# Kernel optimization log

Measured on AMD Instinct MI355X. Metric: run time of the kernel, lower is better.

## Reference

```python
import jax, jax.numpy as jnp
import numpy as np

N = 50000
E = 800000
F_IN = 256
F_OUT = 128
ALPHA = 0.2  # leaky relu negative slope


def setup_inputs() -> dict:
    key = jax.random.key(0)
    k1, k2, k3, k4 = jax.random.split(key, 4)
    x = jax.random.normal(k1, (N, F_IN), dtype=jnp.float32)
    edge_index = jax.random.randint(k2, (2, E), 0, N, dtype=jnp.int64 if jax.config.jax_enable_x64 else jnp.int32)
    # xavier_normal gain=1.414
    W = jax.random.normal(k3, (F_IN, F_OUT), dtype=jnp.float32) * (1.414 * np.sqrt(2.0 / (F_IN + F_OUT)))
    a = jax.random.normal(k4, (2 * F_OUT, 2 * F_OUT), dtype=jnp.float32) * (1.414 * np.sqrt(2.0 / (4 * F_OUT)))
    return {"x": x, "edge_index": edge_index, "W": W, "a": a}


def reference(x, edge_index, W, a):
    n = x.shape[0]
    src = edge_index[0]  # rows of sparse adj
    dst = edge_index[1]  # cols of sparse adj
    h = x @ W  # [N, F_out]
    hs = h[src]  # [E, F_out] gather
    hd = h[dst]  # [E, F_out] gather
    # att_type == 'mx':
    # (a @ edge_h).sum(0) == a.sum(0) @ edge_h where edge_h = cat(hs, hd).T
    asum = a.sum(0)  # [2*F_out]
    lin = hs @ asum[:F_OUT] + hd @ asum[F_OUT:]  # [E]
    conv = (hs * hd).sum(axis=1)  # [E]
    z = lin * jax.nn.sigmoid(conv)
    edge_e = jnp.exp(-jnp.where(z >= 0, z, ALPHA * z))  # exp(-leakyrelu(z))
    # sparse spmm: rowsum (a @ ones) and aggregate (a @ h); dropout p=0 (eval)
    e_rowsum = jax.ops.segment_sum(edge_e, src, num_segments=n) + 1e-8  # [N]
    h_prime = jax.ops.segment_sum(edge_e[:, None] * hd, src, num_segments=n)  # [N, F_out]
    h_prime = h_prime / e_rowsum[:, None]
    return jax.nn.elu(h_prime)  # concat=True
```

## Files before the change

kernel.cpp:

```cpp
#include <hip/hip_runtime.h>

#define NF_IN 256
#define NF 128
#define NEG_SLOPE 0.2f
#define BUCKET 64
#define CAP 12288
#define CH 4096

typedef float f32x4 __attribute__((ext_vector_type(4)));
typedef __bf16 bf16x8 __attribute__((ext_vector_type(8)));
typedef short short8 __attribute__((ext_vector_type(8)));
typedef _Float16 half8 __attribute__((ext_vector_type(8)));
typedef _Float16 half2v __attribute__((ext_vector_type(2)));
struct H2x4 { half2v h[4]; };

__device__ __forceinline__ short bf16_rtne(float f) {
    unsigned u = __float_as_uint(f);
    u += 0x7fffu + ((u >> 16) & 1u);
    return (short)(u >> 16);
}

__global__ __launch_bounds__(256) void stage_pre(const float* __restrict__ a,
                                                 const float* __restrict__ W,
                                                 const int* __restrict__ srcp,
                                                 const int* __restrict__ dstp,
                                                 float* __restrict__ av,
                                                 short* __restrict__ Wt,
                                                 unsigned* __restrict__ gcount,
                                                 unsigned* __restrict__ ebuf,
                                                 int E, int nbuck) {
    __shared__ unsigned pr_pairs[CH];
    __shared__ unsigned pr_ord[CH];
    __shared__ unsigned char pr_bkt[CH];
    __shared__ int pr_hist[128], pr_lstart[128], pr_loff[128], pr_gbase[128];

    const int tid = threadIdx.x;
    const int bid = blockIdx.x;

    if (bid < 8) {
        float s = 0.f;
        const int r0 = bid * 32;
        for (int r = 0; r < 32; ++r) s += a[(size_t)(r0 + r) * (2 * NF) + tid];
        atomicAdd(&av[tid], s);
        return;
    }
    if (bid < 136) {
        const int i = (bid - 8) * 256 + tid;
        const int k = i >> 7, c = i & 127;
        const int t = k >> 5, lg = (k >> 3) & 3, e = k & 7;
        const int q = c >> 4, col = c & 15;
        const float w = W[i];
        const unsigned b = __float_as_uint(w);
        const int base = t * 8192 + q * 512 + lg * 128 + col * 8 + e;
        Wt[base] = (short)(b >> 16);
        Wt[base + 4096] = bf16_rtne(w - __uint_as_float(b & 0xffff0000u));
        return;
    }

    const int e0 = (bid - 136) * CH;
    const int nE = min(CH, E - e0);
    if (nE <= 0) return;

    if (tid < 128) pr_hist[tid] = 0;
    __syncthreads();

    const int nE4 = nE >> 2;
    for (int i = tid; i < nE4; i += 256) {
        const int4 s4 = ((const int4*)(srcp + e0))[i];
        const int4 d4 = ((const int4*)(dstp + e0))[i];
        pr_pairs[i * 4 + 0] = (unsigned)(s4.x & 0xFFFF) | ((unsigned)(d4.x & 0xFFFF) << 16);
        pr_pairs[i * 4 + 1] = (unsigned)(s4.y & 0xFFFF) | ((unsigned)(d4.y & 0xFFFF) << 16);
        pr_pairs[i * 4 + 2] = (unsigned)(s4.z & 0xFFFF) | ((unsigned)(d4.z & 0xFFFF) << 16);
        pr_pairs[i * 4 + 3] = (unsigned)(s4.w & 0xFFFF) | ((unsigned)(d4.w & 0xFFFF) << 16);
        atomicAdd(&pr_hist[s4.x >> 9], 1);
        atomicAdd(&pr_hist[s4.y >> 9], 1);
        atomicAdd(&pr_hist[s4.z >> 9], 1);
        atomicAdd(&pr_hist[s4.w >> 9], 1);
    }
    __syncthreads();

    if (tid == 0) {
        int run = 0;
        for (int b = 0; b < nbuck; ++b) {
            pr_lstart[b] = run;
            pr_loff[b] = run;
            run += pr_hist[b];
        }
    }
    __syncthreads();

    if (tid < nbuck) {
        pr_gbase[tid] = (int)atomicAdd(&gcount[tid], (unsigned)pr_hist[tid]);
        const int st = pr_lstart[tid], cnt = pr_hist[tid];
        for (int j = 0; j < cnt; ++j) pr_bkt[st + j] = (unsigned char)tid;
    }
    __syncthreads();

    for (int i = tid; i < nE; i += 256) {
        const unsigned pv = pr_pairs[i];
        const int b = (int)(pv & 0xFFFF) >> 9;
        const int pos = atomicAdd(&pr_loff[b], 1);
        pr_ord[pos] = pv;
    }
    __syncthreads();

    for (int i = tid; i < nE; i += 256) {
        const int b = pr_bkt[i];
        const long gi = (long)pr_gbase[b] + (i - pr_lstart[b]);
        if (gi < CAP) ebuf[(size_t)b * CAP + gi] = pr_ord[i];
    }
}

__global__ __launch_bounds__(256) void stage_projfill(
        const float* __restrict__ x, const short* __restrict__ Wt,
        const float* __restrict__ av, _Float16* __restrict__ h16,
        float* __restrict__ scs, float* __restrict__ scd, int n, int nProj,
        const unsigned* __restrict__ gcount, const unsigned* __restrict__ ebuf,
        int* __restrict__ deg, unsigned short* __restrict__ nbr) {
    __shared__ short bts[2][8192];

    const int tid = threadIdx.x;

    if (blockIdx.x >= nProj) {
        const int b = blockIdx.x - nProj;
        const int nb0 = b << 9;
        const int nn = min(512, n - nb0);
        if (nn <= 0) return;
        int* deg_l = (int*)&bts[0][0];
        for (int i = tid; i < 512; i += 256) deg_l[i] = 0;

        const unsigned* reg = (const unsigned*)(nbr + ((size_t)nb0 << 6));
        unsigned acc = 0;
        const int words = nn << 5;
        for (int i = tid; i < words; i += 256) acc += reg[i];
        asm volatile("" :: "v"(acc));
        __syncthreads();

        int cnt = (int)gcount[b];
        if (cnt > CAP) cnt = CAP;
        for (int i = tid; i < cnt; i += 256) {
            const unsigned pv = ebuf[(size_t)b * CAP + i];
            const int s = (int)(pv & 0xFFFF);
            const int d = (int)(pv >> 16);
            const int k = atomicAdd(&deg_l[s - nb0], 1);
            if (k < BUCKET) nbr[((size_t)s << 6) + k] = (unsigned short)d;
        }
        __syncthreads();
        for (int i = tid; i < nn; i += 256) deg[nb0 + i] = deg_l[i];
        return;
    }

    const int lane = tid & 63;
    const int wv = tid >> 6;
    const int l15 = lane & 15;
    const int lg = lane >> 4;
    const int rbase = blockIdx.x * 64 + wv * 16;

    int arow = rbase + l15;
    if (arow >= n) arow = n - 1;
    const float* xr = x + (size_t)arow * NF_IN + lg * 8;

    short8 ah[8], al[8];
    #pragma unroll
    for (int t = 0; t < 8; ++t) {
        const float4 u0 = *(const float4*)(xr + t * 32);
        const float4 u1 = *(const float4*)(xr + t * 32 + 4);
        const float xs[8] = {u0.x, u0.y, u0.z, u0.w, u1.x, u1.y, u1.z, u1.w};
        #pragma unroll
        for (int e = 0; e < 8; ++e) {
            const unsigned b = __float_as_uint(xs[e]);
            ah[t][e] = (short)(b >> 16);
            al[t][e] = bf16_rtne(xs[e] - __uint_as_float(b & 0xffff0000u));
        }
    }

    f32x4 acc[8];
    #pragma unroll
    for (int q = 0; q < 8; ++q) acc[q] = (f32x4){0.f, 0.f, 0.f, 0.f};

    #define STAGE(t_, b_)                                                        \
        do {                                                                     \
            const short* gt_ = Wt + (size_t)(t_) * 8192;                         \
            _Pragma("unroll")                                                    \
            for (int i_ = 0; i_ < 4; ++i_) {                                     \
                const int ch_ = wv * 256 + i_ * 64;                              \
                __builtin_amdgcn_global_load_lds(                                \
                    (const __attribute__((address_space(1))) void*)              \
                        (gt_ + (size_t)(ch_ + lane) * 8),                        \
                    (__attribute__((address_space(3))) void*)&bts[b_][ch_ * 8],  \
                    16, 0, 0);                                                   \
            }                                                                    \
        } while (0)

    STAGE(0, 0);

    #pragma unroll
    for (int t = 0; t < 8; ++t) {
        __syncthreads();
        if (t < 7) STAGE(t + 1, (t + 1) & 1);
        const short* Bs = &bts[t & 1][0];
        const int boff = lg * 128 + l15 * 8;
        const bf16x8 ahv = __builtin_bit_cast(bf16x8, ah[t]);
        const bf16x8 alv = __builtin_bit_cast(bf16x8, al[t]);
        #pragma unroll
        for (int q = 0; q < 8; ++q) {
            const short8 bh = *(const short8*)(Bs + q * 512 + boff);
            const short8 bl = *(const short8*)(Bs + 4096 + q * 512 + boff);
            const bf16x8 bhv = __builtin_bit_cast(bf16x8, bh);
            const bf16x8 blv = __builtin_bit_cast(bf16x8, bl);
            acc[q] = __builtin_amdgcn_mfma_f32_16x16x32_bf16(ahv, bhv, acc[q], 0, 0, 0);
            acc[q] = __builtin_amdgcn_mfma_f32_16x16x32_bf16(alv, bhv, acc[q], 0, 0, 0);
            acc[q] = __builtin_amdgcn_mfma_f32_16x16x32_bf16(ahv, blv, acc[q], 0, 0, 0);
        }
    }
    #undef STAGE

    float avA[8], avB[8];
    #pragma unroll
    for (int q = 0; q < 8; ++q) {
        avA[q] = av[q * 16 + l15];
        avB[q] = av[NF + q * 16 + l15];
    }

    #pragma unroll
    for (int r = 0; r < 4; ++r) {
        float ps = 0.f, pd = 0.f;
        #pragma unroll
        for (int q = 0; q < 8; ++q) {
            ps += acc[q][r] * avA[q];
            pd += acc[q][r] * avB[q];
        }
        #pragma unroll
        for (int m_ = 1; m_ <= 8; m_ <<= 1) {
            ps += __shfl_xor(ps, m_, 64);
            pd += __shfl_xor(pd, m_, 64);
        }
        const int row = rbase + lg * 4 + r;
        if (row < n) {
            _Float16* hp = h16 + (size_t)row * NF;
            #pragma unroll
            for (int q = 0; q < 8; ++q) hp[q * 16 + l15] = (_Float16)acc[q][r];
            if (l15 == 0) { scs[row] = ps; scd[row] = pd; }
        }
    }
}

__global__ __launch_bounds__(256) void stage_agg(const _Float16* __restrict__ h16,
                                                 const unsigned short* __restrict__ nbr,
                                                 const int* __restrict__ deg,
                                                 const float* __restrict__ scs,
                                                 const float* __restrict__ scd,
                                                 float* __restrict__ out, int n) {
    const int node = (blockIdx.x * blockDim.x + threadIdx.x) >> 6;
    if (node >= n) return;
    const int lane = threadIdx.x & 63;
    const int qq = lane & 7;
    const int sub = lane >> 3;

    const half8* hself = (const half8*)(h16 + (size_t)node * NF + qq * 16);
    const H2x4 pa0 = __builtin_bit_cast(H2x4, hself[0]);
    const H2x4 pa1 = __builtin_bit_cast(H2x4, hself[1]);

    const float lbase = scs[node];
    const int org = node << 6;
    int dg = deg[node];
    if (dg > BUCKET) dg = BUCKET;

    float t[16];
    #pragma unroll
    for (int e = 0; e < 16; ++e) t[e] = 0.f;
    float zsum = 0.f;

    if (dg > 0) {
        float lA, lB, lC;
        half8 a0, a1, b0, b1, c0, c1;
        {
            const int iA = (int)nbr[org + ((sub < dg) ? sub : 0)];
            lA = scd[iA];
            const half8* hA = (const half8*)(h16 + (size_t)iA * NF + qq * 16);
            a0 = hA[0]; a1 = hA[1];
        }
        lB = 0.f; b0 = a0; b1 = a1;
        if (8 < dg) {
            const int jj = 8 + sub;
            const int iB = (int)nbr[org + ((jj < dg) ? jj : 0)];
            lB = scd[iB];
            const half8* hB = (const half8*)(h16 + (size_t)iB * NF + qq * 16);
            b0 = hB[0]; b1 = hB[1];
        }

        for (int j = 0; j < dg; j += 8) {
            lC = 0.f; c0 = b0; c1 = b1;
            if (j + 16 < dg) {
                const int jj = j + 16 + sub;
                const int iC = (int)nbr[org + ((jj < dg) ? jj : 0)];
                lC = scd[iC];
                const half8* hC = (const half8*)(h16 + (size_t)iC * NF + qq * 16);
                c0 = hC[0]; c1 = hC[1];
            }

            float cv = 0.f;
#if __has_builtin(__builtin_amdgcn_fdot2)
            {
                const H2x4 qa0 = __builtin_bit_cast(H2x4, a0);
                const H2x4 qa1 = __builtin_bit_cast(H2x4, a1);
                #pragma unroll
                for (int i = 0; i < 4; ++i)
                    cv = __builtin_amdgcn_fdot2(pa0.h[i], qa0.h[i], cv, false);
                #pragma unroll
                for (int i = 0; i < 4; ++i)
                    cv = __builtin_amdgcn_fdot2(pa1.h[i], qa1.h[i], cv, false);
            }
#else
            {
                const H2x4 qa0 = __builtin_bit_cast(H2x4, a0);
                const H2x4 qa1 = __builtin_bit_cast(H2x4, a1);
                #pragma unroll
                for (int i = 0; i < 4; ++i) {
                    cv += (float)pa0.h[i][0] * (float)qa0.h[i][0];
                    cv += (float)pa0.h[i][1] * (float)qa0.h[i][1];
                    cv += (float)pa1.h[i][0] * (float)qa1.h[i][0];
                    cv += (float)pa1.h[i][1] * (float)qa1.h[i][1];
                }
            }
#endif
            #pragma unroll
            for (int m = 4; m >= 1; m >>= 1) cv += __shfl_xor(cv, m, 64);

            float qv[16];
            #pragma unroll
            for (int e = 0; e < 8; ++e) { qv[e] = (float)a0[e]; qv[8 + e] = (float)a1[e]; }

            const float gate = 1.0f / (1.0f + __expf(-cv));
            const float zz = (lbase + lA) * gate;
            const float zr = (zz >= 0.f) ? zz : NEG_SLOPE * zz;
            float wt = __expf(-zr);
            if (j + sub >= dg) wt = 0.f;

            #pragma unroll
            for (int e = 0; e < 16; ++e) t[e] += wt * qv[e];
            zsum += wt;

            lA = lB; a0 = b0; a1 = b1;
            lB = lC; b0 = c0; b1 = c1;
        }
    }

    #pragma unroll
    for (int m = 8; m <= 32; m <<= 1) zsum += __shfl_xor(zsum, m, 64);

    const int b0_ = sub & 1, b1_ = (sub >> 1) & 1, b2_ = (sub >> 2) & 1;
    float u[8];
    #pragma unroll
    for (int i = 0; i < 8; ++i) {
        const int alo = ((i >> 1) << 2) | (i & 1);
        const float ka = t[alo], kb = t[alo + 2];
        const float keep = b0_ ? kb : ka;
        const float send = b0_ ? ka : kb;
        u[i] = keep + __shfl_xor(send, 8, 64);
    }
    float v[4];
    #pragma unroll
    for (int j = 0; j < 4; ++j) {
        const int alo = ((j >> 1) << 2) | (j & 1);
        const float ka = u[alo], kb = u[alo + 2];
        const float keep = b1_ ? kb : ka;
        const float send = b1_ ? ka : kb;
        v[j] = keep + __shfl_xor(send, 16, 64);
    }
    float w0, w1;
    {
        const float ka = v[0], kb = v[2];
        const float keep = b2_ ? kb : ka, send = b2_ ? ka : kb;
        w0 = keep + __shfl_xor(send, 32, 64);
    }
    {
        const float ka = v[1], kb = v[3];
        const float keep = b2_ ? kb : ka, send = b2_ ? ka : kb;
        w1 = keep + __shfl_xor(send, 32, 64);
    }

    const float norm = 1.0f / (zsum + 1e-8f);
    float y0 = w0 * norm, y1 = w1 * norm;
    y0 = (y0 > 0.f) ? y0 : (__expf(y0) - 1.f);
    y1 = (y1 > 0.f) ? y1 : (__expf(y1) - 1.f);
    *(float2*)(out + (size_t)node * NF + qq * 16 + sub * 2) = make_float2(y0, y1);
}

extern "C" void kernel_launch(void* const* d_in, const int* in_sizes, int n_in,
                              void* d_out, int out_size, void* d_ws, size_t ws_size,
                              hipStream_t stream) {
    const float* x = (const float*)d_in[0];
    const int* ei = (const int*)d_in[1];
    const float* W = (const float*)d_in[2];
    const float* a = (const float*)d_in[3];
    float* out = (float*)d_out;

    const int n = in_sizes[0] / NF_IN;
    const int E = in_sizes[1] / 2;
    const int* srcp = ei;
    const int* dstp = ei + E;

    char* w = (char*)d_ws;
    _Float16* h16 = (_Float16*)w; w += (size_t)n * NF * 2;
    float* scs = (float*)w;   w += (size_t)n * 4;
    float* scd = (float*)w;   w += (size_t)n * 4;
    float* av = (float*)w;    w += 256 * 4;
    unsigned* gcount = (unsigned*)w; w += 128 * 4;
    int* deg = (int*)w;       w += (size_t)n * 4;
    unsigned short* nbr = (unsigned short*)w; w += (size_t)n * BUCKET * 2;
    short* Wt = (short*)w;    w += (size_t)8 * 8192 * 2 * 2;
    unsigned* ebuf = (unsigned*)w;
    const int nbuck = (n + 511) >> 9;
    w += (size_t)nbuck * CAP * 4;

    const int NB1 = (E + CH - 1) / CH;
    const int nProj = (n + 63) / 64;

    hipMemsetAsync(av, 0, (256 + 128) * 4, stream);

    stage_pre<<<136 + NB1, 256, 0, stream>>>(a, W, srcp, dstp, av, Wt,
                                             gcount, ebuf, E, nbuck);
    stage_projfill<<<nProj + nbuck, 256, 0, stream>>>(
        x, Wt, av, h16, scs, scd, n, nProj, gcount, ebuf, deg, nbr);
    stage_agg<<<((size_t)n * 64 + 255) / 256, 256, 0, stream>>>(h16, nbr, deg, scs, scd,
                                                                out, n);
}
```

Before: 178.0 us.

## Process 16 neighbors per wave iteration with 4 lanes per feature row

The aggregation kernel now assigns 4 lanes per neighbor, each holding 32 fp16 features, so a wave covers 16 neighbors per iteration instead of 8. The 2-deep register prefetch becomes 1-deep, the per-edge dot-product shuffle reduction drops from 3 steps to 2, and the final transpose-reduce gains one extra shuffle level. The intent is to cut loop iterations and per-edge shuffle work for the typical degree of about 16. In exchange each lane holds 32 accumulators plus 64 fp16 inputs, which raises register pressure and can reduce occupancy.

```diff
diff --git a/kernel.cpp b/kernel.cpp
--- a/kernel.cpp
+++ b/kernel.cpp
@@ -254,49 +254,44 @@
     const int node = (blockIdx.x * blockDim.x + threadIdx.x) >> 6;
     if (node >= n) return;
     const int lane = threadIdx.x & 63;
-    const int qq = lane & 7;
-    const int sub = lane >> 3;
-
-    const half8* hself = (const half8*)(h16 + (size_t)node * NF + qq * 16);
+    const int q4 = lane & 3;
+    const int sub = lane >> 2;
+
+    const half8* hself = (const half8*)(h16 + (size_t)node * NF + q4 * 32);
     const H2x4 pa0 = __builtin_bit_cast(H2x4, hself[0]);
     const H2x4 pa1 = __builtin_bit_cast(H2x4, hself[1]);
+    const H2x4 pa2 = __builtin_bit_cast(H2x4, hself[2]);
+    const H2x4 pa3 = __builtin_bit_cast(H2x4, hself[3]);
 
     const float lbase = scs[node];
     const int org = node << 6;
     int dg = deg[node];
     if (dg > BUCKET) dg = BUCKET;
 
-    float t[16];
-    #pragma unroll
-    for (int e = 0; e < 16; ++e) t[e] = 0.f;
+    float t[32];
+    #pragma unroll
+    for (int e = 0; e < 32; ++e) t[e] = 0.f;
     float zsum = 0.f;
 
     if (dg > 0) {
-        float lA, lB, lC;
-        half8 a0, a1, b0, b1, c0, c1;
+        float lA;
+        half8 a0, a1, a2, a3;
         {
             const int iA = (int)nbr[org + ((sub < dg) ? sub : 0)];
             lA = scd[iA];
-            const half8* hA = (const half8*)(h16 + (size_t)iA * NF + qq * 16);
-            a0 = hA[0]; a1 = hA[1];
-        }
-        lB = 0.f; b0 = a0; b1 = a1;
-        if (8 < dg) {
-            const int jj = 8 + sub;
-            const int iB = (int)nbr[org + ((jj < dg) ? jj : 0)];
-            lB = scd[iB];
-            const half8* hB = (const half8*)(h16 + (size_t)iB * NF + qq * 16);
-            b0 = hB[0]; b1 = hB[1];
-        }
-
-        for (int j = 0; j < dg; j += 8) {
-            lC = 0.f; c0 = b0; c1 = b1;
+            const half8* hA = (const half8*)(h16 + (size_t)iA * NF + q4 * 32);
+            a0 = hA[0]; a1 = hA[1]; a2 = hA[2]; a3 = hA[3];
+        }
+
+        for (int j = 0; j < dg; j += 16) {
+            float lB = 0.f;
+            half8 b0 = a0, b1 = a1, b2 = a2, b3 = a3;
             if (j + 16 < dg) {
                 const int jj = j + 16 + sub;
-                const int iC = (int)nbr[org + ((jj < dg) ? jj : 0)];
-                lC = scd[iC];
-                const half8* hC = (const half8*)(h16 + (size_t)iC * NF + qq * 16);
-                c0 = hC[0]; c1 = hC[1];
+                const int iB = (int)nbr[org + ((jj < dg) ? jj : 0)];
+                lB = scd[iB];
+                const half8* hB = (const half8*)(h16 + (size_t)iB * NF + q4 * 32);
+                b0 = hB[0]; b1 = hB[1]; b2 = hB[2]; b3 = hB[3];
             }
 
             float cv = 0.f;
@@ -304,32 +299,37 @@
             {
                 const H2x4 qa0 = __builtin_bit_cast(H2x4, a0);
                 const H2x4 qa1 = __builtin_bit_cast(H2x4, a1);
+                const H2x4 qa2 = __builtin_bit_cast(H2x4, a2);
+                const H2x4 qa3 = __builtin_bit_cast(H2x4, a3);
                 #pragma unroll
-                for (int i = 0; i < 4; ++i)
+                for (int i = 0; i < 4; ++i) {
                     cv = __builtin_amdgcn_fdot2(pa0.h[i], qa0.h[i], cv, false);
-                #pragma unroll
-                for (int i = 0; i < 4; ++i)
                     cv = __builtin_amdgcn_fdot2(pa1.h[i], qa1.h[i], cv, false);
+                    cv = __builtin_amdgcn_fdot2(pa2.h[i], qa2.h[i], cv, false);
+                    cv = __builtin_amdgcn_fdot2(pa3.h[i], qa3.h[i], cv, false);
+                }
             }
 #else
             {
                 const H2x4 qa0 = __builtin_bit_cast(H2x4, a0);
                 const H2x4 qa1 = __builtin_bit_cast(H2x4, a1);
+                const H2x4 qa2 = __builtin_bit_cast(H2x4, a2);
+                const H2x4 qa3 = __builtin_bit_cast(H2x4, a3);
                 #pragma unroll
                 for (int i = 0; i < 4; ++i) {
                     cv += (float)pa0.h[i][0] * (float)qa0.h[i][0];
                     cv += (float)pa0.h[i][1] * (float)qa0.h[i][1];
                     cv += (float)pa1.h[i][0] * (float)qa1.h[i][0];
                     cv += (float)pa1.h[i][1] * (float)qa1.h[i][1];
+                    cv += (float)pa2.h[i][0] * (float)qa2.h[i][0];
+                    cv += (float)pa2.h[i][1] * (float)qa2.h[i][1];
+                    cv += (float)pa3.h[i][0] * (float)qa3.h[i][0];
+                    cv += (float)pa3.h[i][1] * (float)qa3.h[i][1];
                 }
             }
 #endif
-            #pragma unroll
-            for (int m = 4; m >= 1; m >>= 1) cv += __shfl_xor(cv, m, 64);
-
-            float qv[16];
-            #pragma unroll
-            for (int e = 0; e < 8; ++e) { qv[e] = (float)a0[e]; qv[8 + e] = (float)a1[e]; }
+            cv += __shfl_xor(cv, 1, 64);
+            cv += __shfl_xor(cv, 2, 64);
 
             const float gate = 1.0f / (1.0f + __expf(-cv));
             const float zz = (lbase + lA) * gate;
@@ -338,45 +338,58 @@
             if (j + sub >= dg) wt = 0.f;
 
             #pragma unroll
-            for (int e = 0; e < 16; ++e) t[e] += wt * qv[e];
+            for (int e = 0; e < 8; ++e) {
+                t[e]      += wt * (float)a0[e];
+                t[8 + e]  += wt * (float)a1[e];
+                t[16 + e] += wt * (float)a2[e];
+                t[24 + e] += wt * (float)a3[e];
+            }
             zsum += wt;
 
-            lA = lB; a0 = b0; a1 = b1;
-            lB = lC; b0 = c0; b1 = c1;
-        }
-    }
-
-    #pragma unroll
-    for (int m = 8; m <= 32; m <<= 1) zsum += __shfl_xor(zsum, m, 64);
-
-    const int b0_ = sub & 1, b1_ = (sub >> 1) & 1, b2_ = (sub >> 2) & 1;
-    float u[8];
+            lA = lB; a0 = b0; a1 = b1; a2 = b2; a3 = b3;
+        }
+    }
+
+    #pragma unroll
+    for (int m = 4; m <= 32; m <<= 1) zsum += __shfl_xor(zsum, m, 64);
+
+    const int s0 = sub & 1, s1 = (sub >> 1) & 1, s2 = (sub >> 2) & 1, s3 = (sub >> 3) & 1;
+    float u[16];
+    #pragma unroll
+    for (int i = 0; i < 16; ++i) {
+        const int alo = ((i >> 1) << 2) | (i & 1);
+        const float ka = t[alo], kb = t[alo + 2];
+        const float keep = s0 ? kb : ka;
+        const float send = s0 ? ka : kb;
+        u[i] = keep + __shfl_xor(send, 4, 64);
+    }
+    float v[8];
     #pragma unroll
     for (int i = 0; i < 8; ++i) {
         const int alo = ((i >> 1) << 2) | (i & 1);
-        const float ka = t[alo], kb = t[alo + 2];
-        const float keep = b0_ ? kb : ka;
-        const float send = b0_ ? ka : kb;
-        u[i] = keep + __shfl_xor(send, 8, 64);
-    }
-    float v[4];
-    #pragma unroll
-    for (int j = 0; j < 4; ++j) {
-        const int alo = ((j >> 1) << 2) | (j & 1);
         const float ka = u[alo], kb = u[alo + 2];
-        const float keep = b1_ ? kb : ka;
-        const float send = b1_ ? ka : kb;
-        v[j] = keep + __shfl_xor(send, 16, 64);
+        const float keep = s1 ? kb : ka;
+        const float send = s1 ? ka : kb;
+        v[i] = keep + __shfl_xor(send, 8, 64);
+    }
+    float r4_[4];
+    #pragma unroll
+    for (int i = 0; i < 4; ++i) {
+        const int alo = ((i >> 1) << 2) | (i & 1);
+        const float ka = v[alo], kb = v[alo + 2];
+        const float keep = s2 ? kb : ka;
+        const float send = s2 ? ka : kb;
+        r4_[i] = keep + __shfl_xor(send, 16, 64);
     }
     float w0, w1;
     {
-        const float ka = v[0], kb = v[2];
-        const float keep = b2_ ? kb : ka, send = b2_ ? ka : kb;
+        const float ka = r4_[0], kb = r4_[2];
+        const float keep = s3 ? kb : ka, send = s3 ? ka : kb;
         w0 = keep + __shfl_xor(send, 32, 64);
     }
     {
-        const float ka = v[1], kb = v[3];
-        const float keep = b2_ ? kb : ka, send = b2_ ? ka : kb;
+        const float ka = r4_[1], kb = r4_[3];
+        const float keep = s3 ? kb : ka, send = s3 ? ka : kb;
         w1 = keep + __shfl_xor(send, 32, 64);
     }
 
@@ -384,7 +397,7 @@
     float y0 = w0 * norm, y1 = w1 * norm;
     y0 = (y0 > 0.f) ? y0 : (__expf(y0) - 1.f);
     y1 = (y1 > 0.f) ? y1 : (__expf(y1) - 1.f);
-    *(float2*)(out + (size_t)node * NF + qq * 16 + sub * 2) = make_float2(y0, y1);
+    *(float2*)(out + (size_t)node * NF + q4 * 32 + sub * 2) = make_float2(y0, y1);
 }
 
 extern "C" void kernel_launch(void* const* d_in, const int* in_sizes, int n_in,
```

Measured after the change: 183.3 us. 1.03x slower.

## Process two nodes per wavefront in aggregation to interleave independent gathers

Applied to the files above, without the earlier changes.

The aggregation kernel now assigns two destination nodes to each 64-lane wavefront and runs their neighbor loops in lockstep. The two independent gather chains supply memory-level parallelism, replacing the old single-node three-deep prefetch with a two-deep prefetch per node. This costs more registers (two accumulator sets) and adds imbalance when the two nodes' degrees differ. It also halves the number of launched waves.

```diff
diff --git a/kernel.cpp b/kernel.cpp
--- a/kernel.cpp
+++ b/kernel.cpp
@@ -245,146 +245,176 @@
     }
 }
 
+__device__ __forceinline__ void chunk_compute(const H2x4& pa0, const H2x4& pa1,
+                                              const half8& a0, const half8& a1,
+                                              float lA, float lbase, int j, int dg,
+                                              int sub, float t[16], float& zsum) {
+    float cv = 0.f;
+#if __has_builtin(__builtin_amdgcn_fdot2)
+    {
+        const H2x4 qa0 = __builtin_bit_cast(H2x4, a0);
+        const H2x4 qa1 = __builtin_bit_cast(H2x4, a1);
+        #pragma unroll
+        for (int i = 0; i < 4; ++i)
+            cv = __builtin_amdgcn_fdot2(pa0.h[i], qa0.h[i], cv, false);
+        #pragma unroll
+        for (int i = 0; i < 4; ++i)
+            cv = __builtin_amdgcn_fdot2(pa1.h[i], qa1.h[i], cv, false);
+    }
+#else
+    {
+        const H2x4 qa0 = __builtin_bit_cast(H2x4, a0);
+        const H2x4 qa1 = __builtin_bit_cast(H2x4, a1);
+        #pragma unroll
+        for (int i = 0; i < 4; ++i) {
+            cv += (float)pa0.h[i][0] * (float)qa0.h[i][0];
+            cv += (float)pa0.h[i][1] * (float)qa0.h[i][1];
+            cv += (float)pa1.h[i][0] * (float)qa1.h[i][0];
+            cv += (float)pa1.h[i][1] * (float)qa1.h[i][1];
+        }
+    }
+#endif
+    #pragma unroll
+    for (int m = 4; m >= 1; m >>= 1) cv += __shfl_xor(cv, m, 64);
+
+    const float gate = 1.0f / (1.0f + __expf(-cv));
+    const float zz = (lbase + lA) * gate;
+    const float zr = (zz >= 0.f) ? zz : NEG_SLOPE * zz;
+    float wt = __expf(-zr);
+    if (j + sub >= dg) wt = 0.f;
+
+    #pragma unroll
+    for (int e = 0; e < 8; ++e) {
+        t[e]     += wt * (float)a0[e];
+        t[8 + e] += wt * (float)a1[e];
+    }
+    zsum += wt;
+}
+
+__device__ __forceinline__ float2 epilogue16(float t[16], float zsum, int sub) {
+    #pragma unroll
+    for (int m = 8; m <= 32; m <<= 1) zsum += __shfl_xor(zsum, m, 64);
+
+    const int b0_ = sub & 1, b1_ = (sub >> 1) & 1, b2_ = (sub >> 2) & 1;
+    float u[8];
+    #pragma unroll
+    for (int i = 0; i < 8; ++i) {
+        const int alo = ((i >> 1) << 2) | (i & 1);
+        const float ka = t[alo], kb = t[alo + 2];
+        const float keep = b0_ ? kb : ka;
+        const float send = b0_ ? ka : kb;
+        u[i] = keep + __shfl_xor(send, 8, 64);
+    }
+    float v[4];
+    #pragma unroll
+    for (int j = 0; j < 4; ++j) {
+        const int alo = ((j >> 1) << 2) | (j & 1);
+        const float ka = u[alo], kb = u[alo + 2];
+        const float keep = b1_ ? kb : ka;
+        const float send = b1_ ? ka : kb;
+        v[j] = keep + __shfl_xor(send, 16, 64);
+    }
+    float w0, w1;
+    {
+        const float ka = v[0], kb = v[2];
+        const float keep = b2_ ? kb : ka, send = b2_ ? ka : kb;
+        w0 = keep + __shfl_xor(send, 32, 64);
+    }
+    {
+        const float ka = v[1], kb = v[3];
+        const float keep = b2_ ? kb : ka, send = b2_ ? ka : kb;
+        w1 = keep + __shfl_xor(send, 32, 64);
+    }
+
+    const float norm = 1.0f / (zsum + 1e-8f);
+    float y0 = w0 * norm, y1 = w1 * norm;
+    y0 = (y0 > 0.f) ? y0 : (__expf(y0) - 1.f);
+    y1 = (y1 > 0.f) ? y1 : (__expf(y1) - 1.f);
+    return make_float2(y0, y1);
+}
+
 __global__ __launch_bounds__(256) void stage_agg(const _Float16* __restrict__ h16,
                                                  const unsigned short* __restrict__ nbr,
                                                  const int* __restrict__ deg,
                                                  const float* __restrict__ scs,
                                                  const float* __restrict__ scd,
                                                  float* __restrict__ out, int n) {
-    const int node = (blockIdx.x * blockDim.x + threadIdx.x) >> 6;
-    if (node >= n) return;
+    const int wid = (blockIdx.x * blockDim.x + threadIdx.x) >> 6;
+    const int n0 = wid * 2;
+    if (n0 >= n) return;
+    const int n1 = n0 + 1;
+    const bool has1 = (n1 < n);
+    const int n1c = has1 ? n1 : n0;
+
     const int lane = threadIdx.x & 63;
     const int qq = lane & 7;
     const int sub = lane >> 3;
 
-    const half8* hself = (const half8*)(h16 + (size_t)node * NF + qq * 16);
-    const H2x4 pa0 = __builtin_bit_cast(H2x4, hself[0]);
-    const H2x4 pa1 = __builtin_bit_cast(H2x4, hself[1]);
-
-    const float lbase = scs[node];
-    const int org = node << 6;
-    int dg = deg[node];
-    if (dg > BUCKET) dg = BUCKET;
-
-    float t[16];
-    #pragma unroll
-    for (int e = 0; e < 16; ++e) t[e] = 0.f;
-    float zsum = 0.f;
-
-    if (dg > 0) {
-        float lA, lB, lC;
-        half8 a0, a1, b0, b1, c0, c1;
-        {
-            const int iA = (int)nbr[org + ((sub < dg) ? sub : 0)];
-            lA = scd[iA];
-            const half8* hA = (const half8*)(h16 + (size_t)iA * NF + qq * 16);
-            a0 = hA[0]; a1 = hA[1];
-        }
-        lB = 0.f; b0 = a0; b1 = a1;
-        if (8 < dg) {
-            const int jj = 8 + sub;
-            const int iB = (int)nbr[org + ((jj < dg) ? jj : 0)];
-            lB = scd[iB];
+    const half8* hs0 = (const half8*)(h16 + (size_t)n0 * NF + qq * 16);
+    const H2x4 p00 = __builtin_bit_cast(H2x4, hs0[0]);
+    const H2x4 p01 = __builtin_bit_cast(H2x4, hs0[1]);
+    const half8* hs1 = (const half8*)(h16 + (size_t)n1c * NF + qq * 16);
+    const H2x4 p10 = __builtin_bit_cast(H2x4, hs1[0]);
+    const H2x4 p11 = __builtin_bit_cast(H2x4, hs1[1]);
+
+    const float lb0 = scs[n0];
+    const float lb1 = scs[n1c];
+    const int org0 = n0 << 6, org1 = n1c << 6;
+    int dg0 = deg[n0]; if (dg0 > BUCKET) dg0 = BUCKET;
+    int dg1 = has1 ? deg[n1] : 0; if (dg1 > BUCKET) dg1 = BUCKET;
+
+    float t0[16], t1[16];
+    #pragma unroll
+    for (int e = 0; e < 16; ++e) { t0[e] = 0.f; t1[e] = 0.f; }
+    float zs0 = 0.f, zs1 = 0.f;
+
+    float lA0 = 0.f, lA1 = 0.f;
+    half8 a00{}, a01{}, a10{}, a11{};
+    if (dg0 > 0) {
+        const int iA = (int)nbr[org0 + ((sub < dg0) ? sub : 0)];
+        lA0 = scd[iA];
+        const half8* hA = (const half8*)(h16 + (size_t)iA * NF + qq * 16);
+        a00 = hA[0]; a01 = hA[1];
+    }
+    if (dg1 > 0) {
+        const int iA = (int)nbr[org1 + ((sub < dg1) ? sub : 0)];
+        lA1 = scd[iA];
+        const half8* hA = (const half8*)(h16 + (size_t)iA * NF + qq * 16);
+        a10 = hA[0]; a11 = hA[1];
+    }
+
+    const int dgm = (dg0 > dg1) ? dg0 : dg1;
+    for (int j = 0; j < dgm; j += 8) {
+        float lB0 = 0.f; half8 b00 = a00, b01 = a01;
+        if (j + 8 < dg0) {
+            const int jj = j + 8 + sub;
+            const int iB = (int)nbr[org0 + ((jj < dg0) ? jj : 0)];
+            lB0 = scd[iB];
             const half8* hB = (const half8*)(h16 + (size_t)iB * NF + qq * 16);
-            b0 = hB[0]; b1 = hB[1];
-        }
-
-        for (int j = 0; j < dg; j += 8) {
-            lC = 0.f; c0 = b0; c1 = b1;
-            if (j + 16 < dg) {
-                const int jj = j + 16 + sub;
-                const int iC = (int)nbr[org + ((jj < dg) ? jj : 0)];
-                lC = scd[iC];
-                const half8* hC = (const half8*)(h16 + (size_t)iC * NF + qq * 16);
-                c0 = hC[0]; c1 = hC[1];
-            }
-
-            float cv = 0.f;
-#if __has_builtin(__builtin_amdgcn_fdot2)
-            {
-                const H2x4 qa0 = __builtin_bit_cast(H2x4, a0);
-                const H2x4 qa1 = __builtin_bit_cast(H2x4, a1);
-                #pragma unroll
-                for (int i = 0; i < 4; ++i)
-                    cv = __builtin_amdgcn_fdot2(pa0.h[i], qa0.h[i], cv, false);
-                #pragma unroll
-                for (int i = 0; i < 4; ++i)
-                    cv = __builtin_amdgcn_fdot2(pa1.h[i], qa1.h[i], cv, false);
-            }
-#else
-            {
-                const H2x4 qa0 = __builtin_bit_cast(H2x4, a0);
-                const H2x4 qa1 = __builtin_bit_cast(H2x4, a1);
-                #pragma unroll
-                for (int i = 0; i < 4; ++i) {
-                    cv += (float)pa0.h[i][0] * (float)qa0.h[i][0];
-                    cv += (float)pa0.h[i][1] * (float)qa0.h[i][1];
-                    cv += (float)pa1.h[i][0] * (float)qa1.h[i][0];
-                    cv += (float)pa1.h[i][1] * (float)qa1.h[i][1];
-                }
-            }
-#endif
-            #pragma unroll
-            for (int m = 4; m >= 1; m >>= 1) cv += __shfl_xor(cv, m, 64);
-
-            float qv[16];
-            #pragma unroll
-            for (int e = 0; e < 8; ++e) { qv[e] = (float)a0[e]; qv[8 + e] = (float)a1[e]; }
-
-            const float gate = 1.0f / (1.0f + __expf(-cv));
-            const float zz = (lbase + lA) * gate;
-            const float zr = (zz >= 0.f) ? zz : NEG_SLOPE * zz;
-            float wt = __expf(-zr);
-            if (j + sub >= dg) wt = 0.f;
-
-            #pragma unroll
-            for (int e = 0; e < 16; ++e) t[e] += wt * qv[e];
-            zsum += wt;
-
-            lA = lB; a0 = b0; a1 = b1;
-            lB = lC; b0 = c0; b1 = c1;
-        }
-    }
-
-    #pragma unroll
-    for (int m = 8; m <= 32; m <<= 1) zsum += __shfl_xor(zsum, m, 64);
-
-    const int b0_ = sub & 1, b1_ = (sub >> 1) & 1, b2_ = (sub >> 2) & 1;
-    float u[8];
-    #pragma unroll
-    for (int i = 0; i < 8; ++i) {
-        const int alo = ((i >> 1) << 2) | (i & 1);
-        const float ka = t[alo], kb = t[alo + 2];
-        const float keep = b0_ ? kb : ka;
-        const float send = b0_ ? ka : kb;
-        u[i] = keep + __shfl_xor(send, 8, 64);
-    }
-    float v[4];
-    #pragma unroll
-    for (int j = 0; j < 4; ++j) {
-        const int alo = ((j >> 1) << 2) | (j & 1);
-        const float ka = u[alo], kb = u[alo + 2];
-        const float keep = b1_ ? kb : ka;
-        const float send = b1_ ? ka : kb;
-        v[j] = keep + __shfl_xor(send, 16, 64);
-    }
-    float w0, w1;
-    {
-        const float ka = v[0], kb = v[2];
-        const float keep = b2_ ? kb : ka, send = b2_ ? ka : kb;
-        w0 = keep + __shfl_xor(send, 32, 64);
-    }
-    {
-        const float ka = v[1], kb = v[3];
-        const float keep = b2_ ? kb : ka, send = b2_ ? ka : kb;
-        w1 = keep + __shfl_xor(send, 32, 64);
-    }
-
-    const float norm = 1.0f / (zsum + 1e-8f);
-    float y0 = w0 * norm, y1 = w1 * norm;
-    y0 = (y0 > 0.f) ? y0 : (__expf(y0) - 1.f);
-    y1 = (y1 > 0.f) ? y1 : (__expf(y1) - 1.f);
-    *(float2*)(out + (size_t)node * NF + qq * 16 + sub * 2) = make_float2(y0, y1);
+            b00 = hB[0]; b01 = hB[1];
+        }
+        float lB1 = 0.f; half8 b10 = a10, b11 = a11;
+        if (j + 8 < dg1) {
+            const int jj = j + 8 + sub;
+            const int iB = (int)nbr[org1 + ((jj < dg1) ? jj : 0)];
+            lB1 = scd[iB];
+            const half8* hB = (const half8*)(h16 + (size_t)iB * NF + qq * 16);
+            b10 = hB[0]; b11 = hB[1];
+        }
+
+        if (j < dg0) chunk_compute(p00, p01, a00, a01, lA0, lb0, j, dg0, sub, t0, zs0);
+        if (j < dg1) chunk_compute(p10, p11, a10, a11, lA1, lb1, j, dg1, sub, t1, zs1);
+
+        lA0 = lB0; a00 = b00; a01 = b01;
+        lA1 = lB1; a10 = b10; a11 = b11;
+    }
+
+    const float2 y0 = epilogue16(t0, zs0, sub);
+    *(float2*)(out + (size_t)n0 * NF + qq * 16 + sub * 2) = y0;
+    if (has1) {
+        const float2 y1 = epilogue16(t1, zs1, sub);
+        *(float2*)(out + (size_t)n1 * NF + qq * 16 + sub * 2) = y1;
+    }
 }
 
 extern "C" void kernel_launch(void* const* d_in, const int* in_sizes, int n_in,
@@ -423,6 +453,7 @@
                                              gcount, ebuf, E, nbuck);
     stage_projfill<<<nProj + nbuck, 256, 0, stream>>>(
         x, Wt, av, h16, scs, scd, n, nProj, gcount, ebuf, deg, nbr);
-    stage_agg<<<((size_t)n * 64 + 255) / 256, 256, 0, stream>>>(h16, nbr, deg, scs, scd,
-                                                                out, n);
-}
+    const int nPairs = (n + 1) / 2;
+    stage_agg<<<(nPairs * 64 + 255) / 256, 256, 0, stream>>>(h16, nbr, deg, scs, scd,
+                                                             out, n);
+}
```

Result: slower. 184.7 us (+3.8%).
